# Kernel optimization log

Measured on AMD Instinct MI355X. Metric: run time of the kernel, lower is better.

The kernel has to match this reference:

```python
import jax, jax.numpy as jnp
import numpy as np

KS = 3          # deformable kernel size
N = KS * KS     # sampling points per output location


def conv2d(x, w, stride, pad):
    return jax.lax.conv_general_dilated(
        x, w, (stride, stride), [(pad, pad), (pad, pad)],
        dimension_numbers=('NCHW', 'OIHW', 'NCHW'))


def bn_train(x, g, b, eps=1e-5):
    # training-mode BatchNorm2d: per-channel batch statistics (biased var)
    m = jnp.mean(x, axis=(0, 2, 3), keepdims=True)
    v = jnp.var(x, axis=(0, 2, 3), keepdims=True)
    return (x - m) * jax.lax.rsqrt(v + eps) * g.reshape(1, -1, 1, 1) + b.reshape(1, -1, 1, 1)


def gather_xq(xpad, qx, qy):
    # xpad: (b,c,Hp,Wp); qx,qy: (b,h,w,N) int32 -> (b,c,h,w,N)
    b, c, Hp, Wp = xpad.shape
    _, h, w, n = qx.shape
    idx = (qx * Wp + qy).reshape(b, 1, h * w * n)
    xf = xpad.reshape(b, c, Hp * Wp)
    out = jnp.take_along_axis(xf, jnp.broadcast_to(idx, (b, c, h * w * n)), axis=2)
    return out.reshape(b, c, h, w, n)


def deform_conv(x, Wp, bp, Wd):
    # self-contained DeformConv2D (deform-conv-v2 style, no modulation)
    b, c, h, w = x.shape
    offset = conv2d(x, Wp, 1, 1) + bp.reshape(1, -1, 1, 1)      # (b,2N,h,w)
    off = jnp.transpose(offset, (0, 2, 3, 1))                    # (b,h,w,2N)
    xpad = jnp.pad(x, ((0, 0), (0, 0), (1, 1), (1, 1)))          # zero_padding(1)
    Hpad, Wpad = h + 2, w + 2
    r = KS // 2
    pn_x = jnp.repeat(jnp.arange(-r, r + 1, dtype=x.dtype), KS)  # [-1,-1,-1,0,0,0,1,1,1]
    pn_y = jnp.tile(jnp.arange(-r, r + 1, dtype=x.dtype), KS)    # [-1,0,1,...]
    # sampling coords in padded image: p = p0 + pn + offset
    px = off[..., :N] + jnp.arange(1, h + 1, dtype=x.dtype)[None, :, None, None] + pn_x
    py = off[..., N:] + jnp.arange(1, w + 1, dtype=x.dtype)[None, None, :, None] + pn_y
    fx = jnp.floor(jax.lax.stop_gradient(px))
    fy = jnp.floor(jax.lax.stop_gradient(py))
    q_ltx = jnp.clip(fx, 0, Hpad - 1).astype(jnp.int32)
    q_lty = jnp.clip(fy, 0, Wpad - 1).astype(jnp.int32)
    q_rbx = jnp.clip(fx + 1, 0, Hpad - 1).astype(jnp.int32)
    q_rby = jnp.clip(fy + 1, 0, Wpad - 1).astype(jnp.int32)
    pxc = jnp.clip(px, 0, Hpad - 1)
    pyc = jnp.clip(py, 0, Wpad - 1)
    g_lt = (1 + (q_ltx - pxc)) * (1 + (q_lty - pyc))
    g_rb = (1 - (q_rbx - pxc)) * (1 - (q_rby - pyc))
    g_lb = (1 + (q_ltx - pxc)) * (1 - (q_rby - pyc))
    g_rt = (1 - (q_rbx - pxc)) * (1 + (q_lty - pyc))
    x_off = (g_lt[:, None] * gather_xq(xpad, q_ltx, q_lty)
           + g_rb[:, None] * gather_xq(xpad, q_rbx, q_rby)
           + g_lb[:, None] * gather_xq(xpad, q_ltx, q_rby)
           + g_rt[:, None] * gather_xq(xpad, q_rbx, q_lty))    # (b,c,h,w,N)
    # _reshape_x_offset: (b,c,h,w,kx,ky) -> (b,c,h*ks,w*ks)
    x_off = x_off.reshape(b, c, h, w, KS, KS).transpose(0, 1, 2, 4, 3, 5).reshape(b, c, h * KS, w * KS)
    return conv2d(x_off, Wd, KS, 0)                              # stride=ks conv


def setup_inputs() -> dict:
    key = jax.random.key(0)
    ks = jax.random.split(key, 8)
    def w(k, shape, fan):
        return jax.random.normal(k, shape, jnp.float32) * np.float32(1.0 / np.sqrt(fan))
    B = 2048
    return dict(
        x=jax.random.normal(ks[0], (B, 3, 4, 4), jnp.float32),
        W1=w(ks[1], (32, 3, 3, 3), 27),
        g1=jnp.ones(32, jnp.float32), b1=jnp.zeros(32, jnp.float32),
        W2=w(ks[2], (64, 32, 3, 3), 288),
        g2=jnp.ones(64, jnp.float32), b2=jnp.zeros(64, jnp.float32),
        W3=w(ks[3], (128, 64, 3, 3), 576),
        g3=jnp.ones(128, jnp.float32), b3=jnp.zeros(128, jnp.float32),
        Wp=w(ks[4], (18, 128, 3, 3), 1152) * np.float32(0.1),
        bp=jnp.zeros(18, jnp.float32),
        Wd=w(ks[5], (128, 128, 3, 3), 1152),
        g4=jnp.ones(128, jnp.float32), b4=jnp.zeros(128, jnp.float32),
        Wc=w(ks[6], (10, 128), 128),
        bc=jnp.zeros(10, jnp.float32),
    )


def reference(x, W1, g1, b1, W2, g2, b2, W3, g3, b3, Wp, bp, Wd, g4, b4, Wc, bc):
    x = bn_train(jax.nn.relu(conv2d(x, W1, 1, 1)), g1, b1)
    x = bn_train(jax.nn.relu(conv2d(x, W2, 1, 1)), g2, b2)
    x = bn_train(jax.nn.relu(conv2d(x, W3, 1, 1)), g3, b3)
    x = bn_train(jax.nn.relu(deform_conv(x, Wp, bp, Wd)), g4, b4)
    x = jnp.mean(x, axis=(2, 3))  # avg_pool2d(kernel=4) on 4x4 -> 1x1, then flatten
    return x @ Wc.T + bc
```

## Files before the change

kernel.cpp:

```cpp
#include <hip/hip_runtime.h>

#define NB 2048
#define CNT 32768.0f

#define OFF_Y1   0
#define OFF_Y2   1048576
#define OFF_Y3   3145728
#define OFF_MEAN 7340032
#define OFF_ST   11534336
#define OFF_W2P  11536384
#define OFF_W3P  11545600
#define OFF_WPP  11582464
#define OFF_WDP  11600896

typedef __attribute__((ext_vector_type(8))) short bf16x8;
typedef __attribute__((ext_vector_type(4))) float f32x4;

__device__ __forceinline__ unsigned short f2bf(float f) {
  union { float f; unsigned int u; } v; v.f = f;
  unsigned int r = v.u + 0x7FFFu + ((v.u >> 16) & 1u);
  return (unsigned short)(r >> 16);
}

__device__ __forceinline__ void packw_one(const float* __restrict__ w, unsigned short* __restrict__ wpk,
                                          int CI, int CO, int NT, int i) {
  int KST = CI >> 5;
  int j = i & 7, l = (i >> 3) & 63, sn = i >> 9;
  int nt = sn % NT, step = sn / NT;
  int tap = step / KST, ks = step - tap * KST;
  int ci = ks * 32 + (l >> 4) * 8 + j, co = nt * 16 + (l & 15);
  wpk[i] = (co < CO) ? f2bf(w[(co * CI + ci) * 9 + tap]) : (unsigned short)0;
}

__device__ __forceinline__ void packwd_one(const float* __restrict__ Wd, unsigned short* __restrict__ wdp, int i) {
  int co = i / 1152, k = i % 1152;
  int n = k >> 7, ci = k & 127;
  int tt = k >> 5, kk = k & 31, g = kk >> 3, j = kk & 7;
  int nt = co >> 4, cc = co & 15, l = g * 16 + cc;
  wdp[((tt * 8 + nt) * 64 + l) * 8 + j] = f2bf(Wd[co * 1152 + ci * 9 + n]);
}

__global__ __launch_bounds__(256) void k_pre(const float* __restrict__ W2, const float* __restrict__ W3,
                                             const float* __restrict__ Wp, const float* __restrict__ Wd,
                                             unsigned short* __restrict__ w2p, unsigned short* __restrict__ w3p,
                                             unsigned short* __restrict__ wpp, unsigned short* __restrict__ wdp,
                                             const float* __restrict__ x, const float* __restrict__ W1,
                                             float* __restrict__ y1, float* __restrict__ st) {
  __shared__ float xs[192];
  __shared__ float w1s[864];
  __shared__ float sst[64];
  int t = threadIdx.x;
  if (blockIdx.x < 270) {
#pragma unroll
    for (int ii = 0; ii < 4; ++ii) {
      int i = blockIdx.x * 1024 + ii * 256 + t;
      if (i < 18432) packw_one(W2, w2p, 32, 64, 4, i);
      else if (i < 92160) packw_one(W3, w3p, 64, 128, 8, i - 18432);
      else if (i < 129024) packw_one(Wp, wpp, 128, 18, 2, i - 92160);
      else if (i < 276480) packwd_one(Wd, wdp, i - 129024);
    }
    return;
  }
  int b0 = (blockIdx.x - 270) * 4;
  if (t < 192) xs[t] = x[b0 * 48 + t];
  for (int i = t; i < 864; i += 256) w1s[i] = W1[i];
  if (t < 64) sst[t] = 0.f;
  __syncthreads();
  for (int r = 0; r < 2; ++r) {
    int o = t + r * 256;
    int co = o >> 4, p = o & 15, h = p >> 2, w = p & 3;
    float s1 = 0.f, s2 = 0.f;
#pragma unroll
    for (int img = 0; img < 4; ++img) {
      float acc = 0.f;
      for (int ci = 0; ci < 3; ++ci) {
#pragma unroll
        for (int kx = 0; kx < 3; ++kx) {
          int ih = h + kx - 1;
          if (ih < 0 || ih > 3) continue;
#pragma unroll
          for (int ky = 0; ky < 3; ++ky) {
            int iw = w + ky - 1;
            if (iw < 0 || iw > 3) continue;
            acc += w1s[co * 27 + ci * 9 + kx * 3 + ky] * xs[img * 48 + ci * 16 + ih * 4 + iw];
          }
        }
      }
      acc = fmaxf(acc, 0.f);
      y1[(b0 + img) * 512 + o] = acc;
      s1 += acc; s2 += acc * acc;
    }
    atomicAdd(&sst[co], s1);
    atomicAdd(&sst[32 + co], s2);
  }
  __syncthreads();
  if (t < 64) atomicAdd(&st[(t < 32) ? t : (96 + t)], sst[t]);
}

template <int CI, int CO>
__global__ __launch_bounds__(512, 4) void k_convm(const float* __restrict__ yin,
                                                  const unsigned short* __restrict__ wpk,
                                                  const float* __restrict__ stp,
                                                  const float* __restrict__ gp,
                                                  const float* __restrict__ bpar,
                                                  float* __restrict__ yout, float* __restrict__ stout) {
  constexpr int KST = CI / 32, NSTEP = 9 * KST, NT = CO / 16, TPW = NT / 4;
  constexpr int STR = 72;
  __shared__ __align__(16) unsigned short xnT[2][36 * STR];
  __shared__ float cst[2][CO * 16];
  __shared__ float scS[2 * CI];
  __shared__ float sst[2 * CO];
  int b0 = blockIdx.x * 2, t = threadIdx.x;
  uint4 z = {0u, 0u, 0u, 0u};
  for (int i = t; i < (2 * 36 * STR) / 8; i += 512) ((uint4*)xnT)[i] = z;
  if (t < CI) {
    float m = stp[t] / CNT;
    float v = stp[128 + t] / CNT - m * m;
    float s = gp[t] * rsqrtf(fmaxf(v, 0.f) + 1e-5f);
    scS[t] = s; scS[CI + t] = bpar[t] - m * s;
  }
  if (t < 2 * CO) sst[t] = 0.f;
  __syncthreads();
  for (int i = t; i < 2 * CI * 16; i += 512) {
    int img = i / (CI * 16), r = i - img * (CI * 16);
    int c = r >> 4, p = r & 15, h = p >> 2, w = p & 3;
    float v = yin[(b0 + img) * CI * 16 + r] * scS[c] + scS[CI + c];
    xnT[img][((h + 1) * 6 + (w + 1)) * STR + c] = f2bf(v);
  }
  __syncthreads();
  int wv = t >> 6, l = t & 63, px = l & 15, g = l >> 4;
  int h = px >> 2, w = px & 3;
  int img = wv >> 2, wq = wv & 3;
  f32x4 acc[TPW];
#pragma unroll
  for (int tw = 0; tw < TPW; ++tw) acc[tw] = f32x4{0.f, 0.f, 0.f, 0.f};
#pragma unroll
  for (int step = 0; step < NSTEP; ++step) {
    int tap = step / KST, ks = step - tap * KST;
    int kx = tap / 3, ky = tap % 3;
    bf16x8 a = *(const bf16x8*)&xnT[img][((h + kx) * 6 + (w + ky)) * STR + ks * 32 + g * 8];
#pragma unroll
    for (int tw = 0; tw < TPW; ++tw) {
      int nt = wq * TPW + tw;
      bf16x8 bb = *(const bf16x8*)&wpk[((step * NT + nt) * 64 + l) * 8];
      acc[tw] = __builtin_amdgcn_mfma_f32_16x16x32_bf16(a, bb, acc[tw], 0, 0, 0);
    }
  }
  int cc = l & 15;
#pragma unroll
  for (int tw = 0; tw < TPW; ++tw) {
    int co = (wq * TPW + tw) * 16 + cc;
#pragma unroll
    for (int r = 0; r < 4; ++r) cst[img][co * 16 + (g * 4 + r)] = acc[tw][r];
  }
  __syncthreads();
  {
    constexpr int EPT = CO / 16;
    constexpr int TPC = 256 / CO;
    int ime = t >> 8, tl = t & 255;
    int c = tl / TPC, e0 = (tl % TPC) * EPT;
    float s1 = 0.f, s2 = 0.f;
    float vr[EPT];
#pragma unroll
    for (int e = 0; e < EPT; ++e) {
      float v = fmaxf(cst[ime][c * 16 + e0 + e], 0.f);
      vr[e] = v; s1 += v; s2 += v * v;
    }
#pragma unroll
    for (int e = 0; e < EPT; e += 4)
      *(float4*)&yout[(b0 + ime) * CO * 16 + c * 16 + e0 + e] = make_float4(vr[e], vr[e + 1], vr[e + 2], vr[e + 3]);
    atomicAdd(&sst[c], s1);
    atomicAdd(&sst[CO + c], s2);
  }
  __syncthreads();
  if (t < 2 * CO) atomicAdd(&stout[(t < CO) ? t : (128 - CO + t)], sst[t]);
}

__global__ __launch_bounds__(512, 4) void k_deform(const float* __restrict__ y3,
                                                   const unsigned short* __restrict__ wppk,
                                                   const float* __restrict__ bp,
                                                   const unsigned short* __restrict__ wdp,
                                                   const float* __restrict__ stp,
                                                   const float* __restrict__ gp,
                                                   const float* __restrict__ bpar,
                                                   float* __restrict__ meanw, float* __restrict__ stout) {
  __shared__ __align__(16) unsigned char smem[76544];
  unsigned short* xnb2 = (unsigned short*)smem;
  unsigned short* xnT  = (unsigned short*)(smem + 12288);
  unsigned short* sAT  = (unsigned short*)(smem + 12288);
  float* cscr = (float*)(smem + 35328);
  unsigned short* xoffA = (unsigned short*)(smem + 35328);
  float* offs = (float*)(smem + 72192);
  float* scS  = (float*)(smem + 74496);
  float* sst  = (float*)(smem + 75520);
  int b0 = blockIdx.x * 2, t = threadIdx.x;
  uint4 z = {0u, 0u, 0u, 0u};
  for (int i = t; i < 1992; i += 512) ((uint4*)smem)[i] = z;
  if (t < 128) {
    float m = stp[t] / CNT;
    float v = stp[128 + t] / CNT - m * m;
    float s = gp[t] * rsqrtf(fmaxf(v, 0.f) + 1e-5f);
    scS[t] = s; scS[128 + t] = bpar[t] - m * s;
  }
  if (t < 256) sst[t] = 0.f;
  __syncthreads();
  for (int i = t; i < 4096; i += 512) {
    int img = i >> 11, r = i & 2047;
    int c = r >> 4, p = r & 15, h = p >> 2, w = p & 3;
    float v = y3[(b0 + img) * 2048 + r] * scS[c] + scS[128 + c];
    unsigned short bv = f2bf(v);
    xnb2[img * 3072 + c * 24 + p] = bv;
    xnT[img * 4896 + ((h + 1) * 6 + (w + 1)) * 136 + c] = bv;
  }
  __syncthreads();
  int wv = t >> 6, l = t & 63, px = l & 15, g = l >> 4, cc = l & 15;
  int h = px >> 2, w = px & 3;
  {
    int imo = wv >> 2, half = (wv >> 1) & 1, nt = wv & 1;
    f32x4 oa = {0.f, 0.f, 0.f, 0.f};
#pragma unroll
    for (int si = 0; si < 18; ++si) {
      int s2 = half * 18 + si;
      int tap = s2 >> 2, ks = s2 & 3;
      int kx = tap / 3, ky = tap % 3;
      bf16x8 a = *(const bf16x8*)&xnT[imo * 4896 + ((h + kx) * 6 + (w + ky)) * 136 + ks * 32 + g * 8];
      bf16x8 bb = *(const bf16x8*)&wppk[((s2 * 2 + nt) * 64 + l) * 8];
      oa = __builtin_amdgcn_mfma_f32_16x16x32_bf16(a, bb, oa, 0, 0, 0);
    }
#pragma unroll
    for (int r = 0; r < 4; ++r) cscr[wv * 256 + (g * 4 + r) * 16 + px] = oa[r];
  }
  __syncthreads();
  for (int i = t; i < 576; i += 512) {
    int imo = i / 288, r = i - imo * 288;
    int o = r >> 4, pp = r & 15;
    int nt = o >> 4, cc2 = o & 15;
    float v = bp[o] + cscr[(imo * 4 + nt) * 256 + pp * 16 + cc2]
            + cscr[(imo * 4 + 2 + nt) * 256 + pp * 16 + cc2];
    offs[imo * 288 + o * 16 + pp] = v;
  }
  __syncthreads();
  for (int i = t; i < 1440; i += 512) ((uint4*)(smem + 12288))[i] = z;
  __syncthreads();
  if (t < 288) {
    int imo = t / 144, r = t - imo * 144;
    int p = r / 9, n = r % 9;
    int hh = p >> 2, ww = p & 3;
    float sx = offs[imo * 288 + n * 16 + p] + (float)(hh + 1) + (float)(n / 3 - 1);
    float sy = offs[imo * 288 + (9 + n) * 16 + p] + (float)(ww + 1) + (float)(n % 3 - 1);
    float fx = floorf(sx), fy = floorf(sy);
    float qlx = fminf(fmaxf(fx, 0.f), 5.f);
    float qly = fminf(fmaxf(fy, 0.f), 5.f);
    float qrx = fminf(fmaxf(fx + 1.f, 0.f), 5.f);
    float qry = fminf(fmaxf(fy + 1.f, 0.f), 5.f);
    float pxc = fminf(fmaxf(sx, 0.f), 5.f);
    float pyc = fminf(fmaxf(sy, 0.f), 5.f);
    float glt = (1.f + (qlx - pxc)) * (1.f + (qly - pyc));
    float grb = (1.f - (qrx - pxc)) * (1.f - (qry - pyc));
    float glb = (1.f + (qlx - pxc)) * (1.f - (qry - pyc));
    float grt = (1.f - (qrx - pxc)) * (1.f + (qly - pyc));
    int ilx = (int)qlx, ily = (int)qly, irx = (int)qrx, iry = (int)qry;
    int rowb = imo * 5760 + (n * 16 + p) * 40;
    auto PUT = [&](int qx, int qy, float gv) {
      if (qx >= 1 && qx <= 4 && qy >= 1 && qy <= 4)
        sAT[rowb + (qx - 1) * 4 + (qy - 1)] = f2bf(gv);
    };
    PUT(ilx, ily, glt);
    PUT(irx, iry, grb);
    PUT(ilx, iry, glb);
    PUT(irx, ily, grt);
  }
  __syncthreads();
  f32x4 acc0 = {0.f, 0.f, 0.f, 0.f};
  f32x4 acc1 = {0.f, 0.f, 0.f, 0.f};
  for (int ph = 0; ph < 2; ++ph) {
    for (int m = wv; m < 72; m += 8) {
      int imo = m / 36, mm = m - imo * 36;
      int ttl = mm >> 1;
      int tt = ph * 18 + ttl;
      int q = tt & 3, n = tt >> 2;
      int ct = 2 * q + (mm & 1);
      bf16x8 a = *(const bf16x8*)&xnb2[imo * 3072 + (ct * 16 + cc) * 24 + g * 8];
      bf16x8 bS = *(const bf16x8*)&sAT[imo * 5760 + (n * 16 + cc) * 40 + g * 8];
      f32x4 d = __builtin_amdgcn_mfma_f32_16x16x32_bf16(a, bS, f32x4{0.f, 0.f, 0.f, 0.f}, 0, 0, 0);
      int gp2 = (ct & 1) * 2 + (g >> 1);
      unsigned lo = (unsigned)f2bf(d[0]) | ((unsigned)f2bf(d[1]) << 16);
      unsigned hi = (unsigned)f2bf(d[2]) | ((unsigned)f2bf(d[3]) << 16);
      *(uint2*)&xoffA[imo * 9216 + (ttl * 64 + gp2 * 16 + cc) * 8 + (g & 1) * 4] = (uint2){lo, hi};
    }
    __syncthreads();
#pragma unroll
    for (int ti = 0; ti < 18; ++ti) {
      bf16x8 bb = *(const bf16x8*)&wdp[(((ph * 18 + ti) * 8 + wv) * 64 + l) * 8];
      bf16x8 a0 = *(const bf16x8*)&xoffA[(ti * 64 + l) * 8];
      bf16x8 a1 = *(const bf16x8*)&xoffA[9216 + (ti * 64 + l) * 8];
      acc0 = __builtin_amdgcn_mfma_f32_16x16x32_bf16(a0, bb, acc0, 0, 0, 0);
      acc1 = __builtin_amdgcn_mfma_f32_16x16x32_bf16(a1, bb, acc1, 0, 0, 0);
    }
    __syncthreads();
  }
  {
    float s1a = 0.f, s2a = 0.f, s1b = 0.f, s2b = 0.f;
#pragma unroll
    for (int r = 0; r < 4; ++r) {
      float v0 = fmaxf(acc0[r], 0.f);
      float v1 = fmaxf(acc1[r], 0.f);
      s1a += v0; s2a += v0 * v0;
      s1b += v1; s2b += v1 * v1;
    }
    s1a += __shfl_xor(s1a, 16); s1a += __shfl_xor(s1a, 32);
    s2a += __shfl_xor(s2a, 16); s2a += __shfl_xor(s2a, 32);
    s1b += __shfl_xor(s1b, 16); s1b += __shfl_xor(s1b, 32);
    s2b += __shfl_xor(s2b, 16); s2b += __shfl_xor(s2b, 32);
    if (g == 0) {
      int co = wv * 16 + cc;
      meanw[b0 * 128 + co] = s1a;
      meanw[(b0 + 1) * 128 + co] = s1b;
      atomicAdd(&sst[co], s1a + s1b);
      atomicAdd(&sst[128 + co], s2a + s2b);
    }
  }
  __syncthreads();
  if (t < 256) atomicAdd(&stout[t], sst[t]);
}

__global__ __launch_bounds__(256) void k_final(const float* __restrict__ mean,
                                               const float* __restrict__ stp,
                                               const float* __restrict__ gp,
                                               const float* __restrict__ bpar,
                                               const float* __restrict__ Wc, const float* __restrict__ bc,
                                               float* __restrict__ out) {
  __shared__ float wf[1280];
  __shared__ float scS[256];
  __shared__ float tb[10];
  int t = threadIdx.x;
  if (t < 128) {
    float m = stp[t] / CNT;
    float v = stp[128 + t] / CNT - m * m;
    float s = gp[t] * rsqrtf(fmaxf(v, 0.f) + 1e-5f);
    scS[t] = s; scS[128 + t] = bpar[t] - m * s;
  }
  __syncthreads();
  for (int i = t; i < 1280; i += 256) {
    int c = i & 127;
    wf[i] = Wc[i] * scS[c] * 0.0625f;
  }
  __syncthreads();
  if (t < 10) {
    float s = bc[t];
    for (int c = 0; c < 128; ++c) s += Wc[t * 128 + c] * scS[128 + c];
    tb[t] = s;
  }
  __syncthreads();
  int gidx = blockIdx.x * 256 + t;
  int img = gidx / 10, o = gidx - img * 10;
  const float* mr = mean + img * 128;
  const float* wr = wf + o * 128;
  float acc = tb[o];
#pragma unroll 8
  for (int c = 0; c < 128; ++c) acc += wr[c] * mr[c];
  out[gidx] = acc;
}

extern "C" void kernel_launch(void* const* d_in, const int* in_sizes, int n_in,
                              void* d_out, int out_size, void* d_ws, size_t ws_size,
                              hipStream_t stream) {
  const float* x  = (const float*)d_in[0];
  const float* W1 = (const float*)d_in[1];
  const float* g1 = (const float*)d_in[2];
  const float* b1 = (const float*)d_in[3];
  const float* W2 = (const float*)d_in[4];
  const float* g2 = (const float*)d_in[5];
  const float* b2 = (const float*)d_in[6];
  const float* W3 = (const float*)d_in[7];
  const float* g3 = (const float*)d_in[8];
  const float* b3 = (const float*)d_in[9];
  const float* Wp = (const float*)d_in[10];
  const float* bp = (const float*)d_in[11];
  const float* Wd = (const float*)d_in[12];
  const float* g4 = (const float*)d_in[13];
  const float* b4 = (const float*)d_in[14];
  const float* Wc = (const float*)d_in[15];
  const float* bc = (const float*)d_in[16];
  float* ws = (float*)d_ws;
  float* out = (float*)d_out;

  hipMemsetAsync(ws + OFF_ST, 0, 1024 * sizeof(float), stream);
  k_pre<<<782, 256, 0, stream>>>(W2, W3, Wp, Wd,
                                 (unsigned short*)(ws + OFF_W2P), (unsigned short*)(ws + OFF_W3P),
                                 (unsigned short*)(ws + OFF_WPP), (unsigned short*)(ws + OFF_WDP),
                                 x, W1, ws + OFF_Y1, ws + OFF_ST);
  k_convm<32, 64><<<NB / 2, 512, 0, stream>>>(ws + OFF_Y1, (const unsigned short*)(ws + OFF_W2P),
                                              ws + OFF_ST, g1, b1, ws + OFF_Y2, ws + OFF_ST + 256);
  k_convm<64, 128><<<NB / 2, 512, 0, stream>>>(ws + OFF_Y2, (const unsigned short*)(ws + OFF_W3P),
                                               ws + OFF_ST + 256, g2, b2, ws + OFF_Y3, ws + OFF_ST + 512);
  k_deform<<<NB / 2, 512, 0, stream>>>(ws + OFF_Y3, (const unsigned short*)(ws + OFF_WPP), bp,
                                       (const unsigned short*)(ws + OFF_WDP),
                                       ws + OFF_ST + 512, g3, b3, ws + OFF_MEAN, ws + OFF_ST + 768);
  k_final<<<80, 256, 0, stream>>>(ws + OFF_MEAN, ws + OFF_ST + 768, g4, b4, Wc, bc, out);
}
```

Measured before the change: 146.9 us.

## Store intermediate activations as bf16 and process four images per conv block

Intermediate activations y1, y2 and y3 are now written and read as bf16 instead of fp32, halving the global traffic between the conv stages. Batch statistics are still accumulated from the fp32 values before rounding. The conv kernel now handles four images per block. Each wave loads one weight fragment per step and reuses it across two or four images, cutting redundant weight loads. This costs extra LDS, a two-pass epilogue with more barriers, fewer blocks, and an extra bf16 rounding of the stored activations.

```diff
diff --git a/kernel.cpp b/kernel.cpp
--- a/kernel.cpp
+++ b/kernel.cpp
@@ -4,14 +4,14 @@
 #define CNT 32768.0f
 
 #define OFF_Y1   0
-#define OFF_Y2   1048576
-#define OFF_Y3   3145728
-#define OFF_MEAN 7340032
-#define OFF_ST   11534336
-#define OFF_W2P  11536384
-#define OFF_W3P  11545600
-#define OFF_WPP  11582464
-#define OFF_WDP  11600896
+#define OFF_Y2   524288
+#define OFF_Y3   1572864
+#define OFF_MEAN 3670016
+#define OFF_ST   3932160
+#define OFF_W2P  3933184
+#define OFF_W3P  3942400
+#define OFF_WPP  3979264
+#define OFF_WDP  3997696
 
 typedef __attribute__((ext_vector_type(8))) short bf16x8;
 typedef __attribute__((ext_vector_type(4))) float f32x4;
@@ -20,6 +20,10 @@
   union { float f; unsigned int u; } v; v.f = f;
   unsigned int r = v.u + 0x7FFFu + ((v.u >> 16) & 1u);
   return (unsigned short)(r >> 16);
+}
+__device__ __forceinline__ float bf2f(unsigned short u) {
+  union { unsigned int u; float f; } v; v.u = ((unsigned int)u) << 16;
+  return v.f;
 }
 
 __device__ __forceinline__ void packw_one(const float* __restrict__ w, unsigned short* __restrict__ wpk,
@@ -45,7 +49,7 @@
                                              unsigned short* __restrict__ w2p, unsigned short* __restrict__ w3p,
                                              unsigned short* __restrict__ wpp, unsigned short* __restrict__ wdp,
                                              const float* __restrict__ x, const float* __restrict__ W1,
-                                             float* __restrict__ y1, float* __restrict__ st) {
+                                             unsigned short* __restrict__ y1, float* __restrict__ st) {
   __shared__ float xs[192];
   __shared__ float w1s[864];
   __shared__ float sst[64];
@@ -87,7 +91,7 @@
         }
       }
       acc = fmaxf(acc, 0.f);
-      y1[(b0 + img) * 512 + o] = acc;
+      y1[(b0 + img) * 512 + o] = f2bf(acc);
       s1 += acc; s2 += acc * acc;
     }
     atomicAdd(&sst[co], s1);
@@ -98,21 +102,22 @@
 }
 
 template <int CI, int CO>
-__global__ __launch_bounds__(512, 4) void k_convm(const float* __restrict__ yin,
+__global__ __launch_bounds__(512, 4) void k_convm(const unsigned short* __restrict__ yin,
                                                   const unsigned short* __restrict__ wpk,
                                                   const float* __restrict__ stp,
                                                   const float* __restrict__ gp,
                                                   const float* __restrict__ bpar,
-                                                  float* __restrict__ yout, float* __restrict__ stout) {
-  constexpr int KST = CI / 32, NSTEP = 9 * KST, NT = CO / 16, TPW = NT / 4;
-  constexpr int STR = 72;
-  __shared__ __align__(16) unsigned short xnT[2][36 * STR];
+                                                  unsigned short* __restrict__ yout, float* __restrict__ stout) {
+  constexpr int KST = CI / 32, NSTEP = 9 * KST, NT = CO / 16;
+  constexpr int STR = (CI == 64) ? 72 : 40;
+  constexpr int IPW = (CO == 128) ? 4 : 2;
+  __shared__ __align__(16) unsigned short xnT[4][36 * STR];
   __shared__ float cst[2][CO * 16];
   __shared__ float scS[2 * CI];
   __shared__ float sst[2 * CO];
-  int b0 = blockIdx.x * 2, t = threadIdx.x;
+  int b0 = blockIdx.x * 4, t = threadIdx.x;
   uint4 z = {0u, 0u, 0u, 0u};
-  for (int i = t; i < (2 * 36 * STR) / 8; i += 512) ((uint4*)xnT)[i] = z;
+  for (int i = t; i < (4 * 36 * STR) / 8; i += 512) ((uint4*)xnT)[i] = z;
   if (t < CI) {
     float m = stp[t] / CNT;
     float v = stp[128 + t] / CNT - m * m;
@@ -121,62 +126,68 @@
   }
   if (t < 2 * CO) sst[t] = 0.f;
   __syncthreads();
-  for (int i = t; i < 2 * CI * 16; i += 512) {
+  for (int i = t; i < 4 * CI * 16; i += 512) {
     int img = i / (CI * 16), r = i - img * (CI * 16);
     int c = r >> 4, p = r & 15, h = p >> 2, w = p & 3;
-    float v = yin[(b0 + img) * CI * 16 + r] * scS[c] + scS[CI + c];
+    float v = bf2f(yin[(b0 + img) * CI * 16 + r]) * scS[c] + scS[CI + c];
     xnT[img][((h + 1) * 6 + (w + 1)) * STR + c] = f2bf(v);
   }
   __syncthreads();
-  int wv = t >> 6, l = t & 63, px = l & 15, g = l >> 4;
+  int wv = t >> 6, l = t & 63, px = l & 15, g = l >> 4, cc = l & 15;
   int h = px >> 2, w = px & 3;
-  int img = wv >> 2, wq = wv & 3;
-  f32x4 acc[TPW];
-#pragma unroll
-  for (int tw = 0; tw < TPW; ++tw) acc[tw] = f32x4{0.f, 0.f, 0.f, 0.f};
+  int wq = (CO == 128) ? wv : (wv & 3);
+  int ib = (CO == 128) ? 0 : ((wv >> 2) * 2);
+  f32x4 acc[IPW];
+#pragma unroll
+  for (int e = 0; e < IPW; ++e) acc[e] = f32x4{0.f, 0.f, 0.f, 0.f};
 #pragma unroll
   for (int step = 0; step < NSTEP; ++step) {
     int tap = step / KST, ks = step - tap * KST;
     int kx = tap / 3, ky = tap % 3;
-    bf16x8 a = *(const bf16x8*)&xnT[img][((h + kx) * 6 + (w + ky)) * STR + ks * 32 + g * 8];
-#pragma unroll
-    for (int tw = 0; tw < TPW; ++tw) {
-      int nt = wq * TPW + tw;
-      bf16x8 bb = *(const bf16x8*)&wpk[((step * NT + nt) * 64 + l) * 8];
-      acc[tw] = __builtin_amdgcn_mfma_f32_16x16x32_bf16(a, bb, acc[tw], 0, 0, 0);
-    }
-  }
-  int cc = l & 15;
-#pragma unroll
-  for (int tw = 0; tw < TPW; ++tw) {
-    int co = (wq * TPW + tw) * 16 + cc;
-#pragma unroll
-    for (int r = 0; r < 4; ++r) cst[img][co * 16 + (g * 4 + r)] = acc[tw][r];
-  }
-  __syncthreads();
-  {
-    constexpr int EPT = CO / 16;
-    constexpr int TPC = 256 / CO;
-    int ime = t >> 8, tl = t & 255;
-    int c = tl / TPC, e0 = (tl % TPC) * EPT;
-    float s1 = 0.f, s2 = 0.f;
-    float vr[EPT];
-#pragma unroll
-    for (int e = 0; e < EPT; ++e) {
-      float v = fmaxf(cst[ime][c * 16 + e0 + e], 0.f);
-      vr[e] = v; s1 += v; s2 += v * v;
-    }
-#pragma unroll
-    for (int e = 0; e < EPT; e += 4)
-      *(float4*)&yout[(b0 + ime) * CO * 16 + c * 16 + e0 + e] = make_float4(vr[e], vr[e + 1], vr[e + 2], vr[e + 3]);
-    atomicAdd(&sst[c], s1);
-    atomicAdd(&sst[CO + c], s2);
-  }
-  __syncthreads();
+    bf16x8 bb = *(const bf16x8*)&wpk[((step * NT + wq) * 64 + l) * 8];
+    int woff = ((h + kx) * 6 + (w + ky)) * STR + ks * 32 + g * 8;
+#pragma unroll
+    for (int e = 0; e < IPW; ++e) {
+      bf16x8 a = *(const bf16x8*)&xnT[ib + e][woff];
+      acc[e] = __builtin_amdgcn_mfma_f32_16x16x32_bf16(a, bb, acc[e], 0, 0, 0);
+    }
+  }
+  constexpr int EPT = CO / 16;
+  constexpr int TPC = 256 / CO;
+#pragma unroll
+  for (int p = 0; p < 2; ++p) {
+    if (CO == 128 || (wv >> 2) == p) {
+#pragma unroll
+      for (int e = 0; e < 2; ++e) {
+        int src = (CO == 128) ? (2 * p + e) : e;
+        int co = wq * 16 + cc;
+#pragma unroll
+        for (int r = 0; r < 4; ++r) cst[e][co * 16 + (g * 4 + r)] = acc[src][r];
+      }
+    }
+    __syncthreads();
+    {
+      int ime = t >> 8, tl = t & 255;
+      int c = tl / TPC, e0 = (tl % TPC) * EPT;
+      float s1 = 0.f, s2 = 0.f;
+      union { unsigned short u16[8]; uint4 u4; uint2 u2; } pk;
+#pragma unroll
+      for (int e = 0; e < EPT; ++e) {
+        float v = fmaxf(cst[ime][c * 16 + e0 + e], 0.f);
+        pk.u16[e] = f2bf(v);
+        s1 += v; s2 += v * v;
+      }
+      unsigned short* dst = &yout[(b0 + 2 * p + ime) * CO * 16 + c * 16 + e0];
+      if (EPT == 8) *(uint4*)dst = pk.u4; else *(uint2*)dst = pk.u2;
+      atomicAdd(&sst[c], s1);
+      atomicAdd(&sst[CO + c], s2);
+    }
+    __syncthreads();
+  }
   if (t < 2 * CO) atomicAdd(&stout[(t < CO) ? t : (128 - CO + t)], sst[t]);
 }
 
-__global__ __launch_bounds__(512, 4) void k_deform(const float* __restrict__ y3,
+__global__ __launch_bounds__(512, 4) void k_deform(const unsigned short* __restrict__ y3,
                                                    const unsigned short* __restrict__ wppk,
                                                    const float* __restrict__ bp,
                                                    const unsigned short* __restrict__ wdp,
@@ -207,7 +218,7 @@
   for (int i = t; i < 4096; i += 512) {
     int img = i >> 11, r = i & 2047;
     int c = r >> 4, p = r & 15, h = p >> 2, w = p & 3;
-    float v = y3[(b0 + img) * 2048 + r] * scS[c] + scS[128 + c];
+    float v = bf2f(y3[(b0 + img) * 2048 + r]) * scS[c] + scS[128 + c];
     unsigned short bv = f2bf(v);
     xnb2[img * 3072 + c * 24 + p] = bv;
     xnT[img * 4896 + ((h + 1) * 6 + (w + 1)) * 136 + c] = bv;
@@ -389,12 +400,17 @@
   k_pre<<<782, 256, 0, stream>>>(W2, W3, Wp, Wd,
                                  (unsigned short*)(ws + OFF_W2P), (unsigned short*)(ws + OFF_W3P),
                                  (unsigned short*)(ws + OFF_WPP), (unsigned short*)(ws + OFF_WDP),
-                                 x, W1, ws + OFF_Y1, ws + OFF_ST);
-  k_convm<32, 64><<<NB / 2, 512, 0, stream>>>(ws + OFF_Y1, (const unsigned short*)(ws + OFF_W2P),
-                                              ws + OFF_ST, g1, b1, ws + OFF_Y2, ws + OFF_ST + 256);
-  k_convm<64, 128><<<NB / 2, 512, 0, stream>>>(ws + OFF_Y2, (const unsigned short*)(ws + OFF_W3P),
-                                               ws + OFF_ST + 256, g2, b2, ws + OFF_Y3, ws + OFF_ST + 512);
-  k_deform<<<NB / 2, 512, 0, stream>>>(ws + OFF_Y3, (const unsigned short*)(ws + OFF_WPP), bp,
+                                 x, W1, (unsigned short*)(ws + OFF_Y1), ws + OFF_ST);
+  k_convm<32, 64><<<NB / 4, 512, 0, stream>>>((const unsigned short*)(ws + OFF_Y1),
+                                              (const unsigned short*)(ws + OFF_W2P),
+                                              ws + OFF_ST, g1, b1,
+                                              (unsigned short*)(ws + OFF_Y2), ws + OFF_ST + 256);
+  k_convm<64, 128><<<NB / 4, 512, 0, stream>>>((const unsigned short*)(ws + OFF_Y2),
+                                               (const unsigned short*)(ws + OFF_W3P),
+                                               ws + OFF_ST + 256, g2, b2,
+                                               (unsigned short*)(ws + OFF_Y3), ws + OFF_ST + 512);
+  k_deform<<<NB / 2, 512, 0, stream>>>((const unsigned short*)(ws + OFF_Y3),
+                                       (const unsigned short*)(ws + OFF_WPP), bp,
                                        (const unsigned short*)(ws + OFF_WDP),
                                        ws + OFF_ST + 512, g3, b3, ws + OFF_MEAN, ws + OFF_ST + 768);
   k_final<<<80, 256, 0, stream>>>(ws + OFF_MEAN, ws + OFF_ST + 768, g4, b4, Wc, bc, out);
```

After: 124.6 us. 15.2% less time.
